# Optimization experiments

Hardware: AMD Instinct MI355X
Metric: run time of the kernel (lower is better)

Reference implementation:

```python
import jax, jax.numpy as jnp
import numpy as np
import math

DIM = 1024
NUM_HEADS = 16
HEAD_DIM = DIM // NUM_HEADS
ROPE_BASE = 10000.0
LN_EPS = 1e-5


def _rope_tables(seq_len):
    inv_freq = 1.0 / (ROPE_BASE ** (jnp.arange(0, HEAD_DIM, 2, dtype=jnp.float32) / HEAD_DIM))
    t = jnp.arange(seq_len, dtype=jnp.float32)
    freqs = t[:, None] * inv_freq[None, :]            # (T, D/2)
    emb = jnp.concatenate([freqs, freqs], axis=-1)    # (T, D)
    return jnp.cos(emb), jnp.sin(emb)


def _rotate_half(x):
    x1 = x[..., ::2]
    x2 = x[..., 1::2]
    return jnp.stack((-x2, x1), axis=-1).reshape(x.shape)


def _heads(y):
    B, T, _ = y.shape
    return y.reshape(B, T, NUM_HEADS, HEAD_DIM).transpose(0, 2, 1, 3)  # (B,H,T,hd)


def _layernorm(x, w, b):
    mu = jnp.mean(x, axis=-1, keepdims=True)
    var = jnp.var(x, axis=-1, keepdims=True)
    return (x - mu) / jnp.sqrt(var + LN_EPS) * w + b


def setup_inputs() -> dict:
    key = jax.random.key(0)
    ks = jax.random.split(key, 16)
    s = 1.0 / math.sqrt(DIM)
    d = {
        "x": jax.random.normal(ks[0], (2, 2048, DIM), jnp.float32),
        "h_a": jax.random.normal(ks[1], (2, 512, DIM), jnp.float32),
        "h_t": jax.random.normal(ks[2], (2, 64, DIM), jnp.float32),
        "p": jax.random.normal(ks[3], (2, 256, DIM), jnp.float32),
    }
    names = ["Wq", "Wks", "Wvs", "Wka", "Wva", "Wkt", "Wvt", "Wo", "Wf"]
    for i, n in enumerate(names):
        d[n] = jax.random.normal(ks[4 + i], (DIM, DIM), jnp.float32) * s
        d["b" + n[1:]] = jnp.zeros((DIM,), jnp.float32)
    d["gating"] = jnp.zeros((1,), jnp.float32)
    d["ln_w"] = jnp.ones((DIM,), jnp.float32)
    d["ln_b"] = jnp.zeros((DIM,), jnp.float32)
    return d


def reference(x, h_a, h_t, p,
              Wq, bq, Wks, bks, Wvs, bvs, Wka, bka, Wva, bva,
              Wkt, bkt, Wvt, bvt, Wo, bo, Wf, bf,
              gating, ln_w, ln_b):
    B, T, D = x.shape
    g = jnp.tanh(gating)[0]
    h_adapter = jnp.concatenate((h_a, p), axis=1)          # (B, Ta+Tp, D)
    cos, sin = _rope_tables(T)                             # (T, hd)

    q = _heads(x @ Wq + bq)
    ks_ = _heads(x @ Wks + bks)
    vs = _heads(x @ Wvs + bvs)
    q = q * cos + _rotate_half(q) * sin
    ks_ = ks_ * cos + _rotate_half(ks_) * sin

    ka = _heads(h_adapter @ Wka + bka)
    va = _heads(h_adapter @ Wva + bva)
    kt = _heads(h_t @ Wkt + bkt)
    vt = _heads(h_t @ Wvt + bvt)

    s_self = jnp.einsum("bhqd,bhkd->bhqk", q, ks_)
    s_adpt = jnp.einsum("bhqd,bhkd->bhqk", q, ka)
    s_task = jnp.einsum("bhqd,bhkd->bhqk", q, kt) * g
    scores = jnp.concatenate([s_self, s_adpt, s_task], axis=-1) / math.sqrt(HEAD_DIM)
    attn = jax.nn.softmax(scores, axis=-1)                 # (B,H,T,S_total)

    v_all = jnp.concatenate([vs, va, vt], axis=2)          # (B,H,S_total,hd)
    out = jnp.einsum("bhqk,bhkd->bhqd", attn, v_all)
    out = out.transpose(0, 2, 1, 3).reshape(B, T, D)
    out = out @ Wo + bo

    res = _layernorm(out + x, ln_w, ln_b)
    res = jax.nn.relu(res @ Wf + bf)
    return res
```

## Files before the change

### kernel.cpp

```cpp
#include <hip/hip_runtime.h>

typedef __attribute__((ext_vector_type(8))) short bf16x8;
typedef __attribute__((ext_vector_type(4))) float f32x4;
typedef __attribute__((ext_vector_type(8))) unsigned short u16x8;

#define DEV static __device__ __forceinline__

DEV float bf2f(unsigned short u) {
    union { unsigned int i; float f; } x; x.i = ((unsigned int)u) << 16; return x.f;
}
DEV unsigned short f2bf(float f) {
    union { float f; unsigned int i; } x; x.f = f;
    unsigned int r = x.i + 0x7FFFu + ((x.i >> 16) & 1u);
    return (unsigned short)(r >> 16);
}
DEV float ldany(const void* p, size_t i, bool f32) {
    return f32 ? ((const float*)p)[i] : bf2f(((const unsigned short*)p)[i]);
}

struct Quad { const void* w0; const void* w1; const void* w2; const void* w3; };
struct Tri  { const void* b0; const void* b1; const void* b2; void* o0; void* o1; void* o2; };
struct ExtArgs {
    const void* ha; const void* pp; const void* ht;
    const void* bka; const void* bva; const void* bkt; const void* bvt;
    void* kx; void* vx;
};

__global__ __launch_bounds__(64)
void detect_f32(const unsigned int* __restrict__ w, int* __restrict__ flag)
{
    if (threadIdx.x == 0 && blockIdx.x == 0)
        flag[0] = (w[0] == 0x3F800000u) ? 1 : 0;
}

__global__ __launch_bounds__(256)
void transpose_w(Quad q, unsigned short* __restrict__ dstbase, const int* __restrict__ flagp)
{
    const bool dsf = (*flagp != 0);
    const int z = blockIdx.z;
    const void* W = (z == 0) ? q.w0 : (z == 1) ? q.w1 : (z == 2) ? q.w2 : q.w3;
    unsigned short* out = dstbase + ((size_t)z << 20);
    __shared__ unsigned short Ts[64][72];
    const int t = threadIdx.x;
    const int n0 = blockIdx.x * 64, k0 = blockIdx.y * 64;
    const int r = t >> 2, c = (t & 3) << 4;
    if (!dsf) {
        const unsigned short* Wp = (const unsigned short*)W + (size_t)(k0 + r) * 1024 + n0 + c;
        *(u16x8*)&Ts[r][c]     = *(const u16x8*)Wp;
        *(u16x8*)&Ts[r][c + 8] = *(const u16x8*)(Wp + 8);
    } else {
        const float* Wf = (const float*)W + (size_t)(k0 + r) * 1024 + n0 + c;
        #pragma unroll
        for (int j = 0; j < 16; ++j) Ts[r][c + j] = f2bf(Wf[j]);
    }
    __syncthreads();
    unsigned short tmp[16];
    #pragma unroll
    for (int j = 0; j < 16; ++j) tmp[j] = Ts[c + j][r];
    unsigned short* op = out + (size_t)(n0 + r) * 1024 + k0 + c;
    *(u16x8*)op       = *(const u16x8*)&tmp[0];
    *(u16x8*)(op + 8) = *(const u16x8*)&tmp[8];
}

template<int AMODE, int OMODE, bool RELU, bool ROPEF>
__global__ __launch_bounds__(256)
void gemm_mfma(const void* __restrict__ A, const unsigned short* __restrict__ WTbase,
               Tri t3, const int* __restrict__ flagp,
               int mblocks, int rpb_in, int rpb_out, int row_off)
{
    const int K = 1024, N = 1024;
    const bool dsf = (*flagp != 0);
    const bool af32 = (AMODE == 1) && dsf;
    __shared__ unsigned short As[64 * 64];
    __shared__ unsigned short Bs[128 * 64];
    const int tid = threadIdx.x;
    const int z = blockIdx.y / mblocks;
    const int m0 = (blockIdx.y - z * mblocks) * 64;
    const int n0 = blockIdx.x * 128;
    const unsigned short* WT = WTbase + ((size_t)z << 20);
    const void* bias = (z == 0) ? t3.b0 : (z == 1) ? t3.b1 : t3.b2;
    void* Cv = (z == 0) ? t3.o0 : (z == 1) ? t3.o1 : t3.o2;

    const int ar = tid >> 2, aq = (tid & 3) << 1, ah = ar & 7;
    const int br = tid >> 1, bq = (tid & 1) << 2, bh = br & 7;
    const unsigned short* Bg = WT + (size_t)(n0 + br) * K + (bq << 3);
    const size_t arow = (size_t)(m0 + ar) * K + (aq << 3);

    const int lane = tid & 63, wv = tid >> 6;
    const int wm = (wv >> 1) << 5, wn = (wv & 1) << 6;
    const int il = lane & 15, quad = lane >> 4;
    const int h = il & 7;
    const int c0 = ((quad ^ h) << 3);
    int aoff[2], boff[4];
    #pragma unroll
    for (int mi = 0; mi < 2; ++mi) aoff[mi] = (wm + mi * 16 + il) * 64;
    #pragma unroll
    for (int nj = 0; nj < 4; ++nj) boff[nj] = (wn + nj * 16 + il) * 64;

    f32x4 acc[2][4];
    #pragma unroll
    for (int mi = 0; mi < 2; ++mi)
        #pragma unroll
        for (int nj = 0; nj < 4; ++nj) acc[mi][nj] = (f32x4){0.f, 0.f, 0.f, 0.f};

    u16x8 av[2], bv[4];
    auto load_ab = [&](int kq) {
        if (!af32) {
            const unsigned short* Ag = (const unsigned short*)A + arow + kq;
            av[0] = *(const u16x8*)Ag;
            av[1] = *(const u16x8*)(Ag + 8);
        } else {
            const float* Af = (const float*)A + arow + kq;
            #pragma unroll
            for (int j = 0; j < 2; ++j)
                #pragma unroll
                for (int e = 0; e < 8; ++e)
                    ((unsigned short*)&av[j])[e] = f2bf(Af[8 * j + e]);
        }
        #pragma unroll
        for (int j = 0; j < 4; ++j) bv[j] = *(const u16x8*)(Bg + kq + 8 * j);
    };
    load_ab(0);

    for (int k0 = 0; k0 < K; k0 += 64) {
        __syncthreads();
        *(u16x8*)&As[ar * 64 + ((aq ^ ah) << 3)]       = av[0];
        *(u16x8*)&As[ar * 64 + (((aq ^ 1) ^ ah) << 3)] = av[1];
        #pragma unroll
        for (int j = 0; j < 4; ++j)
            *(u16x8*)&Bs[br * 64 + (((bq ^ j) ^ bh) << 3)] = bv[j];
        __syncthreads();
        load_ab((k0 + 64 < K) ? k0 + 64 : k0);
        #pragma unroll
        for (int kk = 0; kk < 2; ++kk) {
            const int cc = c0 ^ (kk << 5);
            bf16x8 af[2], bfr[4];
            #pragma unroll
            for (int mi = 0; mi < 2; ++mi) af[mi] = *(const bf16x8*)&As[aoff[mi] + cc];
            #pragma unroll
            for (int nj = 0; nj < 4; ++nj) bfr[nj] = *(const bf16x8*)&Bs[boff[nj] + cc];
            #pragma unroll
            for (int mi = 0; mi < 2; ++mi)
                #pragma unroll
                for (int nj = 0; nj < 4; ++nj)
                    acc[mi][nj] = __builtin_amdgcn_mfma_f32_16x16x32_bf16(
                        af[mi], bfr[nj], acc[mi][nj], 0, 0, 0);
        }
    }

    const bool doRope = ROPEF && (z < 2);
    float bval[4];
    #pragma unroll
    for (int nj = 0; nj < 4; ++nj) bval[nj] = ldany(bias, n0 + wn + nj * 16 + il, dsf);
    #pragma unroll
    for (int mi = 0; mi < 2; ++mi) {
        #pragma unroll
        for (int r = 0; r < 4; ++r) {
            const int m = m0 + wm + mi * 16 + quad * 4 + r;
            const int bidx = m / rpb_in;
            const size_t orow = (size_t)bidx * rpb_out + row_off + (m - bidx * rpb_in);
            #pragma unroll
            for (int nj = 0; nj < 4; ++nj) {
                float v = acc[mi][nj][r] + bval[nj];
                if (doRope) {
                    const int dcol = n0 + wn + nj * 16 + il;
                    const float a = (float)(m & 2047) *
                        exp2f(-(float)(dcol & 31) * 0.41524101186092033f);
                    float sn, cs;
                    sincosf(a, &sn, &cs);
                    const float partner = __shfl_xor(v, 1);
                    v = (il & 1) ? fmaf(v, cs, partner * sn)
                                 : fmaf(v, cs, -partner * sn);
                }
                if (RELU) v = fmaxf(v, 0.0f);
                const size_t idx = orow * N + n0 + wn + nj * 16 + il;
                if (OMODE == 0) ((unsigned short*)Cv)[idx] = f2bf(v);
                else {
                    if (dsf) ((float*)Cv)[idx] = v;
                    else     ((unsigned short*)Cv)[idx] = f2bf(v);
                }
            }
        }
    }
}

__global__ __launch_bounds__(256)
void gemm_ext(ExtArgs ea, const unsigned short* __restrict__ WTbase,
              const int* __restrict__ flagp)
{
    const int K = 1024, N = 1024;
    const bool dsf = (*flagp != 0);
    __shared__ unsigned short As[64 * 64];
    __shared__ unsigned short Bs[128 * 64];
    const int tid = threadIdx.x;
    const int y = blockIdx.y;
    const int w = (y >= 26) ? 1 : 0;
    const int yy = y - w * 26;
    int s, m0b;
    if (yy < 16)      { s = 0; m0b = yy; }
    else if (yy < 24) { s = 1; m0b = yy - 16; }
    else              { s = 2; m0b = yy - 24; }
    const void* A = (s == 0) ? ea.ha : (s == 1) ? ea.pp : ea.ht;
    const int rpb_in  = (s == 0) ? 512 : (s == 1) ? 256 : 64;
    const int row_off = (s == 0) ? 0 : (s == 1) ? 512 : 768;
    const int wtslot = ((s == 2) ? 2 : 0) + w;
    const void* bias = (w == 0) ? ((s == 2) ? ea.bkt : ea.bka)
                                : ((s == 2) ? ea.bvt : ea.bva);
    void* Cv = (w == 0) ? ea.kx : ea.vx;
    const int m0 = m0b * 64;
    const int n0 = blockIdx.x * 128;
    const unsigned short* WT = WTbase + ((size_t)wtslot << 20);

    const int ar = tid >> 2, aq = (tid & 3) << 1, ah = ar & 7;
    const int br = tid >> 1, bq = (tid & 1) << 2, bh = br & 7;
    const unsigned short* Bg = WT + (size_t)(n0 + br) * K + (bq << 3);
    const size_t arow = (size_t)(m0 + ar) * K + (aq << 3);

    const int lane = tid & 63, wv = tid >> 6;
    const int wm = (wv >> 1) << 5, wn = (wv & 1) << 6;
    const int il = lane & 15, quad = lane >> 4;
    const int h = il & 7;
    const int c0 = ((quad ^ h) << 3);
    int aoff[2], boff[4];
    #pragma unroll
    for (int mi = 0; mi < 2; ++mi) aoff[mi] = (wm + mi * 16 + il) * 64;
    #pragma unroll
    for (int nj = 0; nj < 4; ++nj) boff[nj] = (wn + nj * 16 + il) * 64;

    f32x4 acc[2][4];
    #pragma unroll
    for (int mi = 0; mi < 2; ++mi)
        #pragma unroll
        for (int nj = 0; nj < 4; ++nj) acc[mi][nj] = (f32x4){0.f, 0.f, 0.f, 0.f};

    u16x8 av[2], bv[4];
    auto load_ab = [&](int kq) {
        if (!dsf) {
            const unsigned short* Ag = (const unsigned short*)A + arow + kq;
            av[0] = *(const u16x8*)Ag;
            av[1] = *(const u16x8*)(Ag + 8);
        } else {
            const float* Af = (const float*)A + arow + kq;
            #pragma unroll
            for (int j = 0; j < 2; ++j)
                #pragma unroll
                for (int e = 0; e < 8; ++e)
                    ((unsigned short*)&av[j])[e] = f2bf(Af[8 * j + e]);
        }
        #pragma unroll
        for (int j = 0; j < 4; ++j) bv[j] = *(const u16x8*)(Bg + kq + 8 * j);
    };
    load_ab(0);

    for (int k0 = 0; k0 < K; k0 += 64) {
        __syncthreads();
        *(u16x8*)&As[ar * 64 + ((aq ^ ah) << 3)]       = av[0];
        *(u16x8*)&As[ar * 64 + (((aq ^ 1) ^ ah) << 3)] = av[1];
        #pragma unroll
        for (int j = 0; j < 4; ++j)
            *(u16x8*)&Bs[br * 64 + (((bq ^ j) ^ bh) << 3)] = bv[j];
        __syncthreads();
        load_ab((k0 + 64 < K) ? k0 + 64 : k0);
        #pragma unroll
        for (int kk = 0; kk < 2; ++kk) {
            const int cc = c0 ^ (kk << 5);
            bf16x8 af[2], bfr[4];
            #pragma unroll
            for (int mi = 0; mi < 2; ++mi) af[mi] = *(const bf16x8*)&As[aoff[mi] + cc];
            #pragma unroll
            for (int nj = 0; nj < 4; ++nj) bfr[nj] = *(const bf16x8*)&Bs[boff[nj] + cc];
            #pragma unroll
            for (int mi = 0; mi < 2; ++mi)
                #pragma unroll
                for (int nj = 0; nj < 4; ++nj)
                    acc[mi][nj] = __builtin_amdgcn_mfma_f32_16x16x32_bf16(
                        af[mi], bfr[nj], acc[mi][nj], 0, 0, 0);
        }
    }

    float bval[4];
    #pragma unroll
    for (int nj = 0; nj < 4; ++nj) bval[nj] = ldany(bias, n0 + wn + nj * 16 + il, dsf);
    #pragma unroll
    for (int mi = 0; mi < 2; ++mi) {
        #pragma unroll
        for (int r = 0; r < 4; ++r) {
            const int m = m0 + wm + mi * 16 + quad * 4 + r;
            const int bidx = m / rpb_in;
            const size_t orow = (size_t)bidx * 832 + row_off + (m - bidx * rpb_in);
            #pragma unroll
            for (int nj = 0; nj < 4; ++nj) {
                const float v = acc[mi][nj][r] + bval[nj];
                ((unsigned short*)Cv)[orow * N + n0 + wn + nj * 16 + il] = f2bf(v);
            }
        }
    }
}

__global__ __launch_bounds__(256)
void attn_mfma(const unsigned short* __restrict__ Q, const unsigned short* __restrict__ Ksf,
               const unsigned short* __restrict__ Vsf, const unsigned short* __restrict__ Kx,
               const unsigned short* __restrict__ Vx, const void* __restrict__ gate,
               const int* __restrict__ flagp, unsigned short* __restrict__ AO)
{
    const int T = 2048, TX = 832, D = 1024;
    __shared__ unsigned short lds[2][9216];
    const int tid = threadIdx.x;
    const int bh = blockIdx.x;
    const int b = bh >> 4, h = bh & 15;
    const int t0 = blockIdx.y << 6;
    const bool dsf = (*flagp != 0);
    const float g = tanhf(ldany(gate, 0, dsf));

    const int lane = tid & 63, wv = tid >> 6;
    const int il = lane & 15, quad = lane >> 4;
    const int qw = t0 + (wv << 4);

    bf16x8 qf[2];
    {
        const unsigned short* qp = Q + (size_t)(b * T + qw + il) * D + (h << 6) + quad * 8;
        qf[0] = *(const bf16x8*)qp;
        qf[1] = *(const bf16x8*)(qp + 32);
    }

    const int ksr = tid >> 2, ksd = (tid & 3) << 4;
    const int vkey = tid & 63, vdb = (tid >> 6) << 4;
    const int vpos = (vkey & 15) * 4 + (vkey >> 4);

    float lsum[4] = {0.f, 0.f, 0.f, 0.f};
    f32x4 o[4];
    #pragma unroll
    for (int dt = 0; dt < 4; ++dt) o[dt] = (f32x4){0.f, 0.f, 0.f, 0.f};

    u16x8 kr0, kr1, vr0, vr1;
    auto load_kv = [&](int kt) {
        const unsigned short *kp, *vp;
        if (kt < 32) {
            kp = Ksf + (size_t)(b * T + (kt << 6) + ksr) * D + (h << 6) + ksd;
            vp = Vsf + (size_t)(b * T + (kt << 6) + vkey) * D + (h << 6) + vdb;
        } else {
            kp = Kx + (size_t)(b * TX + ((kt - 32) << 6) + ksr) * D + (h << 6) + ksd;
            vp = Vx + (size_t)(b * TX + ((kt - 32) << 6) + vkey) * D + (h << 6) + vdb;
        }
        kr0 = *(const u16x8*)kp; kr1 = *(const u16x8*)(kp + 8);
        vr0 = *(const u16x8*)vp; vr1 = *(const u16x8*)(vp + 8);
    };
    load_kv(0);

    #pragma unroll 1
    for (int kt = 0; kt < 45; ++kt) {
        const int cur = kt & 1;
        unsigned short* Kl = &lds[cur][0];
        unsigned short* Vl = &lds[cur][4608];
        unsigned short* Pl = &lds[1 - cur][wv * 1152];
        *(u16x8*)&Kl[ksr * 72 + ksd]     = kr0;
        *(u16x8*)&Kl[ksr * 72 + ksd + 8] = kr1;
        #pragma unroll
        for (int j = 0; j < 8; ++j)
            Vl[(vdb + j) * 72 + vpos]     = ((unsigned short*)&vr0)[j];
        #pragma unroll
        for (int j = 0; j < 8; ++j)
            Vl[(vdb + 8 + j) * 72 + vpos] = ((unsigned short*)&vr1)[j];
        __syncthreads();
        if (kt < 44) load_kv(kt + 1);

        f32x4 s[4];
        #pragma unroll
        for (int ct = 0; ct < 4; ++ct) s[ct] = (f32x4){0.f, 0.f, 0.f, 0.f};
        #pragma unroll
        for (int ct = 0; ct < 4; ++ct)
            #pragma unroll
            for (int c = 0; c < 2; ++c) {
                bf16x8 kf = *(const bf16x8*)&Kl[(ct * 16 + il) * 72 + c * 32 + quad * 8];
                s[ct] = __builtin_amdgcn_mfma_f32_16x16x32_bf16(qf[c], kf, s[ct], 0, 0, 0);
            }
        const float fc = ((kt == 44) ? g : 1.0f) * 0.18033688011112042f;

        #pragma unroll
        for (int r = 0; r < 4; ++r) {
            const float e0 = exp2f(fmaf(s[0][r], fc, -11.541560327111708f));
            const float e1 = exp2f(fmaf(s[1][r], fc, -11.541560327111708f));
            const float e2 = exp2f(fmaf(s[2][r], fc, -11.541560327111708f));
            const float e3 = exp2f(fmaf(s[3][r], fc, -11.541560327111708f));
            lsum[r] += (e0 + e1) + (e2 + e3);
            const unsigned int lo =
                (__float_as_uint(e1) & 0xFFFF0000u) | (__float_as_uint(e0) >> 16);
            const unsigned int hi =
                (__float_as_uint(e3) & 0xFFFF0000u) | (__float_as_uint(e2) >> 16);
            *(uint2*)&Pl[(quad * 4 + r) * 72 + (il << 2)] = make_uint2(lo, hi);
        }

        #pragma unroll
        for (int c = 0; c < 2; ++c) {
            bf16x8 pf = *(const bf16x8*)&Pl[il * 72 + c * 32 + quad * 8];
            #pragma unroll
            for (int dt = 0; dt < 4; ++dt) {
                bf16x8 vf = *(const bf16x8*)&Vl[(dt * 16 + il) * 72 + c * 32 + quad * 8];
                o[dt] = __builtin_amdgcn_mfma_f32_16x16x32_bf16(pf, vf, o[dt], 0, 0, 0);
            }
        }
        __syncthreads();
    }

    #pragma unroll
    for (int r = 0; r < 4; ++r) {
        float t = lsum[r];
        #pragma unroll
        for (int off = 1; off <= 8; off <<= 1) t += __shfl_xor(t, off);
        lsum[r] = 1.0f / t;
    }
    #pragma unroll
    for (int dt = 0; dt < 4; ++dt)
        #pragma unroll
        for (int r = 0; r < 4; ++r)
            AO[(size_t)(b * T + qw + quad * 4 + r) * D + (h << 6) + dt * 16 + il] =
                f2bf(o[dt][r] * lsum[r]);
}

__global__ __launch_bounds__(256)
void ln_res(const unsigned short* __restrict__ proj, const void* __restrict__ x,
            const void* __restrict__ w, const void* __restrict__ bb,
            const int* __restrict__ flagp, unsigned short* __restrict__ y)
{
    const int row = blockIdx.x;
    const int tid = threadIdx.x;
    const bool dsf = (*flagp != 0);
    const unsigned short* pr = proj + (size_t)row * 1024;
    float v[4];
    #pragma unroll
    for (int e = 0; e < 4; ++e)
        v[e] = bf2f(pr[(tid << 2) + e]) + ldany(x, (size_t)row * 1024 + (tid << 2) + e, dsf);
    float s1 = v[0] + v[1] + v[2] + v[3];
    float s2 = v[0]*v[0] + v[1]*v[1] + v[2]*v[2] + v[3]*v[3];
    #pragma unroll
    for (int off = 1; off < 64; off <<= 1) {
        s1 += __shfl_xor(s1, off);
        s2 += __shfl_xor(s2, off);
    }
    __shared__ float red1[4], red2[4];
    const int wv = tid >> 6;
    if ((tid & 63) == 0) { red1[wv] = s1; red2[wv] = s2; }
    __syncthreads();
    s1 = red1[0] + red1[1] + red1[2] + red1[3];
    s2 = red2[0] + red2[1] + red2[2] + red2[3];
    const float mu = s1 * (1.0f / 1024.0f);
    const float var = s2 * (1.0f / 1024.0f) - mu * mu;
    const float rstd = rsqrtf(var + 1e-5f);
    #pragma unroll
    for (int e = 0; e < 4; ++e) {
        const int d = (tid << 2) + e;
        const float yy = (v[e] - mu) * rstd * ldany(w, d, dsf) + ldany(bb, d, dsf);
        y[(size_t)row * 1024 + d] = f2bf(yy);
    }
}

extern "C" void kernel_launch(void* const* d_in, const int* in_sizes, int n_in,
                              void* d_out, int out_size, void* d_ws, size_t ws_size,
                              hipStream_t stream)
{
    const void* x    = d_in[0];
    const void* h_a  = d_in[1];
    const void* h_t  = d_in[2];
    const void* p    = d_in[3];
    const void* Wq   = d_in[4];
    const void* bq   = d_in[5];
    const void* Wks  = d_in[6];
    const void* bks  = d_in[7];
    const void* Wvs  = d_in[8];
    const void* bvs  = d_in[9];
    const void* Wka  = d_in[10];
    const void* bka  = d_in[11];
    const void* Wva  = d_in[12];
    const void* bva  = d_in[13];
    const void* Wkt  = d_in[14];
    const void* bkt  = d_in[15];
    const void* Wvt  = d_in[16];
    const void* bvt  = d_in[17];
    const void* Wo   = d_in[18];
    const void* bo   = d_in[19];
    const void* Wf   = d_in[20];
    const void* bf_  = d_in[21];
    const void* gating = d_in[22];
    const void* ln_w = d_in[23];
    const void* ln_b = d_in[24];

    char* ws = (char*)d_ws;
    int*            flag = (int*)ws;
    unsigned short* qb   = (unsigned short*)(ws + 256);
    unsigned short* ks   = (unsigned short*)(ws + 8388864);
    unsigned short* vs   = (unsigned short*)(ws + 16777472);
    unsigned short* kx   = (unsigned short*)(ws + 25166080);
    unsigned short* vx   = (unsigned short*)(ws + 28573952);
    unsigned short* ao   = (unsigned short*)(ws + 31981824);
    unsigned short* proj  = ks;
    unsigned short* lnout = vs;
    unsigned short* WT1 = ao;
    unsigned short* WT3 = kx;

    dim3 blk(256);
    const Tri nul = {};

    detect_f32<<<1, 64, 0, stream>>>((const unsigned int*)ln_w, flag);

    transpose_w<<<dim3(16, 16, 3), blk, 0, stream>>>(Quad{Wq, Wks, Wvs, Wvs}, WT1, flag);
    {
        Tri t3 = {bq, bks, bvs, qb, ks, vs};
        gemm_mfma<1, 0, false, true><<<dim3(8, 64 * 3), blk, 0, stream>>>(
            x, WT1, t3, flag, 64, 4096, 4096, 0);
    }

    transpose_w<<<dim3(16, 16, 4), blk, 0, stream>>>(Quad{Wka, Wva, Wkt, Wvt}, WT1, flag);
    {
        ExtArgs ea = {h_a, p, h_t, bka, bva, bkt, bvt, kx, vx};
        gemm_ext<<<dim3(8, 52), blk, 0, stream>>>(ea, WT1, flag);
    }

    attn_mfma<<<dim3(32, 32), blk, 0, stream>>>(qb, ks, vs, kx, vx, gating, flag, ao);

    transpose_w<<<dim3(16, 16, 2), blk, 0, stream>>>(Quad{Wo, Wf, Wf, Wf}, WT3, flag);
    {
        Tri t3 = {bo, nul.b1, nul.b2, proj, nul.o1, nul.o2};
        gemm_mfma<0, 0, false, false><<<dim3(8, 64), blk, 0, stream>>>(
            ao, WT3, t3, flag, 64, 4096, 4096, 0);
    }
    ln_res<<<4096, blk, 0, stream>>>(proj, x, ln_w, ln_b, flag, lnout);
    {
        Tri t3 = {bf_, nul.b1, nul.b2, d_out, nul.o1, nul.o2};
        gemm_mfma<0, 2, true, false><<<dim3(8, 64), blk, 0, stream>>>(
            lnout, WT3 + ((size_t)1 << 20), t3, flag, 64, 4096, 4096, 0);
    }
}
```

Before: 401.0 us.

## Process 32 query rows per wave in attention, compute row sums via MFMA

Each attention workgroup now handles 128 query rows (32 per wave, two 16-row MFMA tiles), so every K/V tile loaded into LDS is reused across twice as many queries and the grid halves. The softmax denominator is accumulated with an MFMA against a vector of ones instead of scalar adds plus a final shuffle reduction. P gets its own LDS buffers, and the trailing __syncthreads in the loop is removed, relying on K/V double buffering. Register pressure rises with doubled accumulators, and with only 512 blocks occupancy drops. Dropping the end-of-iteration barrier may allow a race on the K/V buffer that is rewritten two iterations later.

```diff
diff --git a/kernel.cpp b/kernel.cpp
--- a/kernel.cpp
+++ b/kernel.cpp
@@ -304,33 +304,43 @@
                const int* __restrict__ flagp, unsigned short* __restrict__ AO)
 {
     const int T = 2048, TX = 832, D = 1024;
-    __shared__ unsigned short lds[2][9216];
+    __shared__ unsigned short Klds[2][64 * 72];
+    __shared__ unsigned short Vlds[2][64 * 72];
+    __shared__ unsigned short Plds[4][32 * 72];
     const int tid = threadIdx.x;
     const int bh = blockIdx.x;
     const int b = bh >> 4, h = bh & 15;
-    const int t0 = blockIdx.y << 6;
+    const int t0 = blockIdx.y << 7;
     const bool dsf = (*flagp != 0);
     const float g = tanhf(ldany(gate, 0, dsf));
 
     const int lane = tid & 63, wv = tid >> 6;
     const int il = lane & 15, quad = lane >> 4;
-    const int qw = t0 + (wv << 4);
-
-    bf16x8 qf[2];
-    {
-        const unsigned short* qp = Q + (size_t)(b * T + qw + il) * D + (h << 6) + quad * 8;
-        qf[0] = *(const bf16x8*)qp;
-        qf[1] = *(const bf16x8*)(qp + 32);
-    }
+    const int qw = t0 + (wv << 5);
+
+    bf16x8 qf[2][2];
+    #pragma unroll
+    for (int mi = 0; mi < 2; ++mi) {
+        const unsigned short* qp =
+            Q + (size_t)(b * T + qw + mi * 16 + il) * D + (h << 6) + quad * 8;
+        qf[mi][0] = *(const bf16x8*)qp;
+        qf[mi][1] = *(const bf16x8*)(qp + 32);
+    }
+    bf16x8 ones;
+    #pragma unroll
+    for (int e = 0; e < 8; ++e) ((unsigned short*)&ones)[e] = 0x3F80;
 
     const int ksr = tid >> 2, ksd = (tid & 3) << 4;
     const int vkey = tid & 63, vdb = (tid >> 6) << 4;
     const int vpos = (vkey & 15) * 4 + (vkey >> 4);
 
-    float lsum[4] = {0.f, 0.f, 0.f, 0.f};
-    f32x4 o[4];
-    #pragma unroll
-    for (int dt = 0; dt < 4; ++dt) o[dt] = (f32x4){0.f, 0.f, 0.f, 0.f};
+    f32x4 o[2][4], ol[2];
+    #pragma unroll
+    for (int mi = 0; mi < 2; ++mi) {
+        ol[mi] = (f32x4){0.f, 0.f, 0.f, 0.f};
+        #pragma unroll
+        for (int dt = 0; dt < 4; ++dt) o[mi][dt] = (f32x4){0.f, 0.f, 0.f, 0.f};
+    }
 
     u16x8 kr0, kr1, vr0, vr1;
     auto load_kv = [&](int kt) {
@@ -350,71 +360,83 @@
     #pragma unroll 1
     for (int kt = 0; kt < 45; ++kt) {
         const int cur = kt & 1;
-        unsigned short* Kl = &lds[cur][0];
-        unsigned short* Vl = &lds[cur][4608];
-        unsigned short* Pl = &lds[1 - cur][wv * 1152];
-        *(u16x8*)&Kl[ksr * 72 + ksd]     = kr0;
-        *(u16x8*)&Kl[ksr * 72 + ksd + 8] = kr1;
+        *(u16x8*)&Klds[cur][ksr * 72 + ksd]     = kr0;
+        *(u16x8*)&Klds[cur][ksr * 72 + ksd + 8] = kr1;
         #pragma unroll
         for (int j = 0; j < 8; ++j)
-            Vl[(vdb + j) * 72 + vpos]     = ((unsigned short*)&vr0)[j];
+            Vlds[cur][(vdb + j) * 72 + vpos]     = ((unsigned short*)&vr0)[j];
         #pragma unroll
         for (int j = 0; j < 8; ++j)
-            Vl[(vdb + 8 + j) * 72 + vpos] = ((unsigned short*)&vr1)[j];
+            Vlds[cur][(vdb + 8 + j) * 72 + vpos] = ((unsigned short*)&vr1)[j];
         __syncthreads();
         if (kt < 44) load_kv(kt + 1);
 
-        f32x4 s[4];
-        #pragma unroll
-        for (int ct = 0; ct < 4; ++ct) s[ct] = (f32x4){0.f, 0.f, 0.f, 0.f};
-        #pragma unroll
-        for (int ct = 0; ct < 4; ++ct)
+        f32x4 s[2][4];
+        #pragma unroll
+        for (int mi = 0; mi < 2; ++mi)
+            #pragma unroll
+            for (int ct = 0; ct < 4; ++ct) s[mi][ct] = (f32x4){0.f, 0.f, 0.f, 0.f};
+        #pragma unroll
+        for (int ct = 0; ct < 4; ++ct) {
             #pragma unroll
             for (int c = 0; c < 2; ++c) {
-                bf16x8 kf = *(const bf16x8*)&Kl[(ct * 16 + il) * 72 + c * 32 + quad * 8];
-                s[ct] = __builtin_amdgcn_mfma_f32_16x16x32_bf16(qf[c], kf, s[ct], 0, 0, 0);
+                bf16x8 kf = *(const bf16x8*)&Klds[cur][(ct * 16 + il) * 72 + c * 32 + quad * 8];
+                #pragma unroll
+                for (int mi = 0; mi < 2; ++mi)
+                    s[mi][ct] = __builtin_amdgcn_mfma_f32_16x16x32_bf16(
+                        qf[mi][c], kf, s[mi][ct], 0, 0, 0);
             }
+        }
         const float fc = ((kt == 44) ? g : 1.0f) * 0.18033688011112042f;
 
         #pragma unroll
-        for (int r = 0; r < 4; ++r) {
-            const float e0 = exp2f(fmaf(s[0][r], fc, -11.541560327111708f));
-            const float e1 = exp2f(fmaf(s[1][r], fc, -11.541560327111708f));
-            const float e2 = exp2f(fmaf(s[2][r], fc, -11.541560327111708f));
-            const float e3 = exp2f(fmaf(s[3][r], fc, -11.541560327111708f));
-            lsum[r] += (e0 + e1) + (e2 + e3);
-            const unsigned int lo =
-                (__float_as_uint(e1) & 0xFFFF0000u) | (__float_as_uint(e0) >> 16);
-            const unsigned int hi =
-                (__float_as_uint(e3) & 0xFFFF0000u) | (__float_as_uint(e2) >> 16);
-            *(uint2*)&Pl[(quad * 4 + r) * 72 + (il << 2)] = make_uint2(lo, hi);
-        }
+        for (int mi = 0; mi < 2; ++mi)
+            #pragma unroll
+            for (int r = 0; r < 4; ++r) {
+                const float e0 = exp2f(fmaf(s[mi][0][r], fc, -11.541560327111708f));
+                const float e1 = exp2f(fmaf(s[mi][1][r], fc, -11.541560327111708f));
+                const float e2 = exp2f(fmaf(s[mi][2][r], fc, -11.541560327111708f));
+                const float e3 = exp2f(fmaf(s[mi][3][r], fc, -11.541560327111708f));
+                const unsigned int lo =
+                    (__float_as_uint(e1) & 0xFFFF0000u) | (__float_as_uint(e0) >> 16);
+                const unsigned int hi =
+                    (__float_as_uint(e3) & 0xFFFF0000u) | (__float_as_uint(e2) >> 16);
+                *(uint2*)&Plds[wv][(mi * 16 + quad * 4 + r) * 72 + (il << 2)] =
+                    make_uint2(lo, hi);
+            }
 
         #pragma unroll
         for (int c = 0; c < 2; ++c) {
-            bf16x8 pf = *(const bf16x8*)&Pl[il * 72 + c * 32 + quad * 8];
+            bf16x8 pf[2];
+            #pragma unroll
+            for (int mi = 0; mi < 2; ++mi)
+                pf[mi] = *(const bf16x8*)&Plds[wv][(mi * 16 + il) * 72 + c * 32 + quad * 8];
+            #pragma unroll
+            for (int mi = 0; mi < 2; ++mi)
+                ol[mi] = __builtin_amdgcn_mfma_f32_16x16x32_bf16(pf[mi], ones, ol[mi], 0, 0, 0);
             #pragma unroll
             for (int dt = 0; dt < 4; ++dt) {
-                bf16x8 vf = *(const bf16x8*)&Vl[(dt * 16 + il) * 72 + c * 32 + quad * 8];
-                o[dt] = __builtin_amdgcn_mfma_f32_16x16x32_bf16(pf, vf, o[dt], 0, 0, 0);
+                bf16x8 vf = *(const bf16x8*)&Vlds[cur][(dt * 16 + il) * 72 + c * 32 + quad * 8];
+                #pragma unroll
+                for (int mi = 0; mi < 2; ++mi)
+                    o[mi][dt] = __builtin_amdgcn_mfma_f32_16x16x32_bf16(
+                        pf[mi], vf, o[mi][dt], 0, 0, 0);
             }
         }
-        __syncthreads();
-    }
-
-    #pragma unroll
-    for (int r = 0; r < 4; ++r) {
-        float t = lsum[r];
-        #pragma unroll
-        for (int off = 1; off <= 8; off <<= 1) t += __shfl_xor(t, off);
-        lsum[r] = 1.0f / t;
-    }
-    #pragma unroll
-    for (int dt = 0; dt < 4; ++dt)
-        #pragma unroll
-        for (int r = 0; r < 4; ++r)
-            AO[(size_t)(b * T + qw + quad * 4 + r) * D + (h << 6) + dt * 16 + il] =
-                f2bf(o[dt][r] * lsum[r]);
+    }
+
+    #pragma unroll
+    for (int mi = 0; mi < 2; ++mi) {
+        float invl[4];
+        #pragma unroll
+        for (int r = 0; r < 4; ++r) invl[r] = 1.0f / ol[mi][r];
+        #pragma unroll
+        for (int dt = 0; dt < 4; ++dt)
+            #pragma unroll
+            for (int r = 0; r < 4; ++r)
+                AO[(size_t)(b * T + qw + mi * 16 + quad * 4 + r) * D + (h << 6) + dt * 16 + il] =
+                    f2bf(o[mi][dt][r] * invl[r]);
+    }
 }
 
 __global__ __launch_bounds__(256)
@@ -515,7 +537,7 @@
         gemm_ext<<<dim3(8, 52), blk, 0, stream>>>(ea, WT1, flag);
     }
 
-    attn_mfma<<<dim3(32, 32), blk, 0, stream>>>(qb, ks, vs, kx, vx, gating, flag, ao);
+    attn_mfma<<<dim3(32, 16), blk, 0, stream>>>(qb, ks, vs, kx, vx, gating, flag, ao);
 
     transpose_w<<<dim3(16, 16, 2), blk, 0, stream>>>(Quad{Wo, Wf, Wf, Wf}, WT3, flag);
     {
```

Measured after the change: 384.7 us. 1.04x faster.
